# Optimization experiments

Hardware: AMD Instinct MI355X
Metric: run time of the kernel (lower is better)

Reference implementation:

```python
import jax, jax.numpy as jnp
import numpy as np

# BEV geometric-kernel-attention shapes
SPATIAL = np.array([[92, 160], [46, 80], [23, 40], [12, 20]], dtype=np.int64)
LEVEL_START = np.concatenate([[0], np.cumsum(SPATIAL[:, 0] * SPATIAL[:, 1])[:-1]]).astype(np.int64)
NUM_VALUE = int((SPATIAL[:, 0] * SPATIAL[:, 1]).sum())  # 19560
B, NQ, H, L, P, D = 1, 20000, 8, 4, 8, 32


def setup_inputs() -> dict:
    key = jax.random.key(0)
    k1, k2, k3 = jax.random.split(key, 3)
    value = jax.random.normal(k1, (B, NUM_VALUE, H, D), dtype=jnp.float32)
    sampling_locations = jax.random.uniform(k2, (B, NQ, H, L, P, 2), dtype=jnp.float32)
    attention_weights = jax.random.uniform(k3, (B, NQ, H, L, P), dtype=jnp.float32)
    attention_weights = attention_weights / attention_weights.sum(axis=(-2, -1), keepdims=True)
    return {
        "value": value,
        "spatial_shapes": jnp.asarray(SPATIAL),
        "level_start_index": jnp.asarray(LEVEL_START),
        "sampling_locations": sampling_locations,
        "attention_weights": attention_weights,
    }


def _gka(value, spatial_shapes, level_start_index, sampling_locations, attention_weights):
    # value: [B, Nv, H, D]; locations: [B, Nq, H, L, P, 2] normalized to [0,1]
    b, nv, h, d = value.shape
    nq, l, p = sampling_locations.shape[1], sampling_locations.shape[3], sampling_locations.shape[4]
    Hs = spatial_shapes[:, 0]  # [L]
    Ws = spatial_shapes[:, 1]
    x = sampling_locations[..., 0]  # [B,Nq,H,L,P]
    y = sampling_locations[..., 1]
    # GKT: nearest/integer (geometric) sampling: floor(loc * size)
    col = jnp.floor(x * Ws[None, None, None, :, None].astype(x.dtype)).astype(jnp.int32)
    row = jnp.floor(y * Hs[None, None, None, :, None].astype(y.dtype)).astype(jnp.int32)
    valid = (col >= 0) & (col < Ws[None, None, None, :, None]) & \
            (row >= 0) & (row < Hs[None, None, None, :, None])
    flat = level_start_index[None, None, None, :, None] + row * Ws[None, None, None, :, None] + col
    flat = jnp.clip(flat, 0, nv - 1)  # [B,Nq,H,L,P] int
    # gather per (batch, head): value_t [B,H,Nv,D]
    v = jnp.transpose(value, (0, 2, 1, 3))
    idx = jnp.transpose(flat, (0, 2, 1, 3, 4)).reshape(b, h, nq * l * p)
    sampled = jnp.take_along_axis(v, idx[..., None], axis=2)  # [B,H,Nq*L*P,D]
    sampled = sampled.reshape(b, h, nq, l, p, d)
    w = jnp.transpose(attention_weights, (0, 2, 1, 3, 4)) * \
        jnp.transpose(valid, (0, 2, 1, 3, 4)).astype(attention_weights.dtype)  # [B,H,Nq,L,P]
    out = jnp.einsum('bhqlp,bhqlpd->bhqd', w, sampled)  # weighted reduce over levels/points
    return jnp.transpose(out, (0, 2, 1, 3)).reshape(b, nq, h * d)


def reference(value, spatial_shapes, level_start_index, sampling_locations, attention_weights):
    out = _gka(value, spatial_shapes, level_start_index, sampling_locations, attention_weights)
    # module returns (output1, output2) from Func and FuncLoad variants — identical math
    return (out, out)
```

## Files before the change

kernel.cpp:

```cpp
#include <hip/hip_runtime.h>


#define GKA_NQ       20000
#define GKA_H        8
#define GKA_NV       19560
#define GKA_OUT_HALF 5120000

__global__ __launch_bounds__(256) void gka_kernel(
    const float* __restrict__ value,
    const float* __restrict__ sloc,
    const float* __restrict__ awgt,
    float* __restrict__ out)
{
    const int tid  = threadIdx.x;
    const int lane = tid & 63;
    const int wave = tid >> 6;
    const int h      = blockIdx.x & 7;
    const int qchunk = blockIdx.x >> 3;
    const int qq   = lane >> 3;
    const int sub  = lane & 7;
    const int q    = qchunk * 32 + wave * 8 + qq;

    const int lvl = sub >> 1;
    const int Wi  = (lvl == 0) ? 160 : (lvl == 1) ? 80 : (lvl == 2) ? 40 : 20;
    const int Hi  = (lvl == 0) ? 92  : (lvl == 1) ? 46 : (lvl == 2) ? 23 : 12;
    const int ls  = (lvl == 0) ? 0   : (lvl == 1) ? 14720 : (lvl == 2) ? 18400 : 19320;
    const float Wf = (float)Wi;
    const float Hf = (float)Hi;

    const int qh = q * GKA_H + h;
    const float4* lp = (const float4*)(sloc + (size_t)qh * 64 + sub * 8);
    const float4 xy0 = lp[0];
    const float4 xy1 = lp[1];
    const float4 w4  = *(const float4*)(awgt + (size_t)qh * 32 + sub * 4);

    int   fl[4];
    float wk[4];
    {
        const float xs[4] = {xy0.x, xy0.z, xy1.x, xy1.z};
        const float ys[4] = {xy0.y, xy0.w, xy1.y, xy1.w};
        const float ws[4] = {w4.x, w4.y, w4.z, w4.w};
        #pragma unroll
        for (int k = 0; k < 4; ++k) {
            const int col = (int)floorf(xs[k] * Wf);
            const int row = (int)floorf(ys[k] * Hf);
            const bool valid = (col >= 0) & (col < Wi) & (row >= 0) & (row < Hi);
            int f = ls + row * Wi + col;
            f = min(max(f, 0), GKA_NV - 1);
            fl[k] = f;
            wk[k] = valid ? ws[k] : 0.0f;
        }
    }

    float4 acc = make_float4(0.f, 0.f, 0.f, 0.f);
    const float* vbase = value + h * 32 + sub * 4;
    const int gbase = lane & 56;
    #pragma unroll
    for (int j = 0; j < 32; ++j) {
        const int src = gbase | (j >> 2);
        const int   f = __shfl(fl[j & 3], src, 64);
        const float w = __shfl(wk[j & 3], src, 64);
        const float4 v = *(const float4*)(vbase + (size_t)f * 256);
        acc.x = fmaf(w, v.x, acc.x);
        acc.y = fmaf(w, v.y, acc.y);
        acc.z = fmaf(w, v.z, acc.z);
        acc.w = fmaf(w, v.w, acc.w);
    }

    float* o = out + (size_t)q * 256 + h * 32 + sub * 4;
    *(float4*)o = acc;
    *(float4*)(o + GKA_OUT_HALF) = acc;
}

extern "C" void kernel_launch(void* const* d_in, const int* in_sizes, int n_in,
                              void* d_out, int out_size, void* d_ws, size_t ws_size,
                              hipStream_t stream) {
    const float* value = (const float*)d_in[0];
    const float* sloc  = (const float*)d_in[3];
    const float* awgt  = (const float*)d_in[4];
    float* out = (float*)d_out;

    dim3 grid((GKA_NQ / 32) * GKA_H);
    gka_kernel<<<grid, 256, 0, stream>>>(value, sloc, awgt, out);
}
```

Measured before the change: 44.51 us.

## Stage coarse-level value rows in LDS as bf16 and enlarge blocks

Each 1024-thread block first copies the level 2 and level 3 value rows for its head into shared memory, converted to bf16. Those levels' gathers then read from LDS instead of global memory, while levels 0 and 1 still gather from global. Queries per block rise from 32 to 128 to spread the staging cost, with a tail guard on the query index. This adds per-block staging work and a barrier, and it lowers precision for half of the samples.

New measurement: 50.23 us. +12.9%, slower.

```diff
diff --git a/kernel.cpp b/kernel.cpp
--- a/kernel.cpp
+++ b/kernel.cpp
@@ -4,22 +4,49 @@
 #define GKA_NQ       20000
 #define GKA_H        8
 #define GKA_NV       19560
+#define GKA_L23BASE  18400
+#define GKA_L23ROWS  1160
 #define GKA_OUT_HALF 5120000
 
-__global__ __launch_bounds__(256) void gka_kernel(
+static __device__ __forceinline__ unsigned short f2bf(float x) {
+    unsigned u = __float_as_uint(x);
+    unsigned r = 0x7FFFu + ((u >> 16) & 1u);
+    return (unsigned short)((u + r) >> 16);
+}
+static __device__ __forceinline__ float bf2f(unsigned short b) {
+    return __uint_as_float(((unsigned)b) << 16);
+}
+
+__global__ __launch_bounds__(1024) void gka_kernel(
     const float* __restrict__ value,
     const float* __restrict__ sloc,
     const float* __restrict__ awgt,
     float* __restrict__ out)
 {
-    const int tid  = threadIdx.x;
+    __shared__ ushort vlds[GKA_L23ROWS * 32];
+
+    const int tid   = threadIdx.x;
+    const int h     = blockIdx.x & 7;
+    const int chunk = blockIdx.x >> 3;
+
+    {
+        const float* src = value + (size_t)GKA_L23BASE * 256 + h * 32;
+        for (int i = tid; i < GKA_L23ROWS * 8; i += 1024) {
+            const int r = i >> 3, c = i & 7;
+            const float4 f = *(const float4*)(src + (size_t)r * 256 + c * 4);
+            ushort4 b;
+            b.x = f2bf(f.x); b.y = f2bf(f.y); b.z = f2bf(f.z); b.w = f2bf(f.w);
+            *(ushort4*)(vlds + i * 4) = b;
+        }
+    }
+
     const int lane = tid & 63;
     const int wave = tid >> 6;
-    const int h      = blockIdx.x & 7;
-    const int qchunk = blockIdx.x >> 3;
     const int qq   = lane >> 3;
     const int sub  = lane & 7;
-    const int q    = qchunk * 32 + wave * 8 + qq;
+    const int qloc = wave * 8 + qq;
+    const int q    = chunk * 128 + qloc;
+    const bool alive = (q < GKA_NQ);
 
     const int lvl = sub >> 1;
     const int Wi  = (lvl == 0) ? 160 : (lvl == 1) ? 80 : (lvl == 2) ? 40 : 20;
@@ -28,15 +55,14 @@
     const float Wf = (float)Wi;
     const float Hf = (float)Hi;
 
-    const int qh = q * GKA_H + h;
-    const float4* lp = (const float4*)(sloc + (size_t)qh * 64 + sub * 8);
-    const float4 xy0 = lp[0];
-    const float4 xy1 = lp[1];
-    const float4 w4  = *(const float4*)(awgt + (size_t)qh * 32 + sub * 4);
-
     int   fl[4];
     float wk[4];
-    {
+    if (alive) {
+        const int qh = q * GKA_H + h;
+        const float4* lp = (const float4*)(sloc + (size_t)qh * 64 + sub * 8);
+        const float4 xy0 = lp[0];
+        const float4 xy1 = lp[1];
+        const float4 w4  = *(const float4*)(awgt + (size_t)qh * 32 + sub * 4);
         const float xs[4] = {xy0.x, xy0.z, xy1.x, xy1.z};
         const float ys[4] = {xy0.y, xy0.w, xy1.y, xy1.w};
         const float ws[4] = {w4.x, w4.y, w4.z, w4.w};
@@ -47,29 +73,50 @@
             const bool valid = (col >= 0) & (col < Wi) & (row >= 0) & (row < Hi);
             int f = ls + row * Wi + col;
             f = min(max(f, 0), GKA_NV - 1);
+            if (sub >= 4)
+                f = min(max(f, GKA_L23BASE), GKA_NV - 1) - GKA_L23BASE;
             fl[k] = f;
             wk[k] = valid ? ws[k] : 0.0f;
         }
+    } else {
+        #pragma unroll
+        for (int k = 0; k < 4; ++k) { fl[k] = 0; wk[k] = 0.0f; }
     }
 
+    __syncthreads();
+
     float4 acc = make_float4(0.f, 0.f, 0.f, 0.f);
-    const float* vbase = value + h * 32 + sub * 4;
     const int gbase = lane & 56;
-    #pragma unroll
-    for (int j = 0; j < 32; ++j) {
-        const int src = gbase | (j >> 2);
-        const int   f = __shfl(fl[j & 3], src, 64);
-        const float w = __shfl(wk[j & 3], src, 64);
-        const float4 v = *(const float4*)(vbase + (size_t)f * 256);
-        acc.x = fmaf(w, v.x, acc.x);
-        acc.y = fmaf(w, v.y, acc.y);
-        acc.z = fmaf(w, v.z, acc.z);
-        acc.w = fmaf(w, v.w, acc.w);
+    if (alive) {
+        const float* vg = value + h * 32 + sub * 4;
+        #pragma unroll
+        for (int j = 0; j < 16; ++j) {
+            const int   s = gbase | (j >> 2);
+            const int   f = __shfl(fl[j & 3], s, 64);
+            const float w = __shfl(wk[j & 3], s, 64);
+            const float4 v = *(const float4*)(vg + (size_t)f * 256);
+            acc.x = fmaf(w, v.x, acc.x);
+            acc.y = fmaf(w, v.y, acc.y);
+            acc.z = fmaf(w, v.z, acc.z);
+            acc.w = fmaf(w, v.w, acc.w);
+        }
+        const ushort* vl = vlds + sub * 4;
+        #pragma unroll
+        for (int j = 16; j < 32; ++j) {
+            const int   s = gbase | (j >> 2);
+            const int   r = __shfl(fl[j & 3], s, 64);
+            const float w = __shfl(wk[j & 3], s, 64);
+            const ushort4 v = *(const ushort4*)(vl + r * 32);
+            acc.x = fmaf(w, bf2f(v.x), acc.x);
+            acc.y = fmaf(w, bf2f(v.y), acc.y);
+            acc.z = fmaf(w, bf2f(v.z), acc.z);
+            acc.w = fmaf(w, bf2f(v.w), acc.w);
+        }
+
+        float* o = out + (size_t)q * 256 + h * 32 + sub * 4;
+        *(float4*)o = acc;
+        *(float4*)(o + GKA_OUT_HALF) = acc;
     }
-
-    float* o = out + (size_t)q * 256 + h * 32 + sub * 4;
-    *(float4*)o = acc;
-    *(float4*)(o + GKA_OUT_HALF) = acc;
 }
 
 extern "C" void kernel_launch(void* const* d_in, const int* in_sizes, int n_in,
@@ -80,6 +127,6 @@
     const float* awgt  = (const float*)d_in[4];
     float* out = (float*)d_out;
 
-    dim3 grid((GKA_NQ / 32) * GKA_H);
-    gka_kernel<<<grid, 256, 0, stream>>>(value, sloc, awgt, out);
+    dim3 grid(157 * GKA_H);
+    gka_kernel<<<grid, 1024, 0, stream>>>(value, sloc, awgt, out);
 }
```
